# Kernel optimization log

Hardware: AMD Instinct MI355X
Metric: run time of the kernel (lower is better)

Reference implementation:

```python
import jax, jax.numpy as jnp
import numpy as np

B, N, D, P = 4, 4096, 64, 2
M, H = 64, 128
ARENA = 20.0  # positions uniform in [0, ARENA]^2; radius 1.0 -> ~32 neighbors


def _mlp2(x, Wa, ba, Wb, bb):
    return jax.nn.relu(x @ Wa + ba) @ Wb + bb


def setup_inputs() -> dict:
    key = jax.random.key(0)
    ks = jax.random.split(key, 14)
    def lin(k, fan_in, fan_out):
        bound = 1.0 / np.sqrt(fan_in)
        kw, kb = jax.random.split(k)
        W = jax.random.uniform(kw, (fan_in, fan_out), jnp.float32, -bound, bound)
        b = jax.random.uniform(kb, (fan_out,), jnp.float32, -bound, bound)
        return W, b
    W1, b1 = lin(ks[0], D, H)
    W2, b2 = lin(ks[1], H, M)
    W3, b3 = lin(ks[2], 2 * M, H)
    W4, b4 = lin(ks[3], H, M)
    W5, b5 = lin(ks[4], D + M, H)
    W6, b6 = lin(ks[5], H, D)
    agent_states = jax.random.normal(ks[6], (B, N, D), jnp.float32)
    agent_positions = jax.random.uniform(ks[7], (B, N, P), jnp.float32) * ARENA
    return {
        "agent_states": agent_states,
        "agent_positions": agent_positions,
        "neighbor_radius": 1,
        "W1": W1, "b1": b1, "W2": W2, "b2": b2,
        "W3": W3, "b3": b3, "W4": W4, "b4": b4,
        "W5": W5, "b5": b5, "W6": W6, "b6": b6,
    }


def reference(agent_states, agent_positions, neighbor_radius,
              W1, b1, W2, b2, W3, b3, W4, b4, W5, b5, W6, b6):
    n = agent_states.shape[1]
    # message encoder MLP: [B,N,D] -> [B,N,M]
    messages = _mlp2(agent_states, W1, b1, W2, b2)
    # dense pairwise distances [B,N,N] (faithful to original O(N^2) mask)
    diff = agent_positions[:, :, None, :] - agent_positions[:, None, :, :]
    distances = jnp.sqrt(jnp.sum(diff * diff, axis=-1))
    adj = (distances < jnp.float32(neighbor_radius)).astype(messages.dtype)
    adj = adj * (1.0 - jnp.eye(n, dtype=messages.dtype))[None]
    deg = jnp.clip(jnp.sum(adj, axis=-1, keepdims=True), 1.0, None)
    adj = adj / deg
    # vectorized form of the per-agent gather-aggregate loop
    aggregated = jnp.einsum('bij,bjm->bim', adj, messages)
    combined = jnp.concatenate([messages, aggregated], axis=-1)
    final_msgs = _mlp2(combined, W3, b3, W4, b4)
    feats = jnp.concatenate([agent_states, final_msgs], axis=-1)
    out = _mlp2(feats, W5, b5, W6, b6)
    return agent_states + out
```

## Files before the change

kernel.cpp:

```cpp
#include <hip/hip_runtime.h>

typedef unsigned short u16;
typedef __bf16 bf16x8 __attribute__((ext_vector_type(8)));
typedef unsigned short ushort8 __attribute__((ext_vector_type(8)));
typedef float f32x4 __attribute__((ext_vector_type(4)));

#define DEV_INLINE __device__ __forceinline__

constexpr int NB = 4;
constexpr int NAG = 4096;
constexpr int ROWS = NB * NAG;
constexpr int GRID = 20;
constexpr int CELLS = GRID * GRID;
constexpr int CSTRIDE = 404;
constexpr int MAXNB = 320;

DEV_INLINE u16 f2bu(float x) { __bf16 h = (__bf16)x; return __builtin_bit_cast(u16, h); }
DEV_INLINE float bu2f(u16 u) { return __builtin_bit_cast(float, ((unsigned)u) << 16); }

DEV_INLINE f32x4 MF(bf16x8 a, const u16* p, f32x4 c) {
  ushort8 bu = *(const ushort8*)p;
  return __builtin_amdgcn_mfma_f32_16x16x32_bf16(a, __builtin_bit_cast(bf16x8, bu), c, 0, 0, 0);
}

template<bool BF>
DEV_INLINE bf16x8 loadA(const void* __restrict__ src, int row, int c) {
  if constexpr (BF) {
    ushort8 u = *reinterpret_cast<const ushort8*>((const u16*)src + (size_t)row * 64 + c);
    return __builtin_bit_cast(bf16x8, u);
  } else {
    const float* f = (const float*)src + (size_t)row * 64 + c;
    f32x4 a = *(const f32x4*)f;
    f32x4 b = *(const f32x4*)(f + 4);
    bf16x8 r;
    r[0] = (__bf16)a[0]; r[1] = (__bf16)a[1]; r[2] = (__bf16)a[2]; r[3] = (__bf16)a[3];
    r[4] = (__bf16)b[0]; r[5] = (__bf16)b[1]; r[6] = (__bf16)b[2]; r[7] = (__bf16)b[3];
    return r;
  }
}

__global__ __launch_bounds__(256) void fused_setup_mlp1(
    const float* __restrict__ pos, const float* __restrict__ states,
    const float* __restrict__ W1, const float* __restrict__ b1,
    const float* __restrict__ W2, const float* __restrict__ b2,
    const float* __restrict__ W3, const float* __restrict__ W4,
    const float* __restrict__ W5, const float* __restrict__ W6,
    u16* __restrict__ wts, u16* __restrict__ msgs,
    float2* __restrict__ pos_sorted, int* __restrict__ cell_start,
    int* __restrict__ sid)
{
  extern __shared__ u16 smem[];
  const int tid = threadIdx.x;
  const int lane = tid & 63;
  const int wave = tid >> 6;

  if (blockIdx.x < NB) {
    int* cnt_s = (int*)smem;
    int* start_s = cnt_s + CELLS;
    u16* cell_of = (u16*)(start_s + CELLS + 1);
    u16* rank_of = cell_of + NAG;
    const int b = blockIdx.x;
    const float2* pb = (const float2*)(pos + (size_t)b * NAG * 2);
    for (int c = tid; c < CELLS; c += 256) cnt_s[c] = 0;
    __syncthreads();
    for (int i = tid; i < NAG; i += 256) {
      float2 p = pb[i];
      int cx = min(max((int)floorf(p.x), 0), GRID - 1);
      int cy = min(max((int)floorf(p.y), 0), GRID - 1);
      int c = cy * GRID + cx;
      rank_of[i] = (u16)atomicAdd(&cnt_s[c], 1);
      cell_of[i] = (u16)c;
    }
    __syncthreads();
    if (wave == 0) {
      int carry = 0;
      for (int g = 0; g < CELLS; g += 64) {
        int c = g + lane;
        int x = (c < CELLS) ? cnt_s[c] : 0;
#pragma unroll
        for (int off = 1; off < 64; off <<= 1) {
          int y = __shfl_up(x, off, 64);
          if (lane >= off) x += y;
        }
        if (c < CELLS) start_s[c + 1] = carry + x;
        carry += __shfl(x, 63, 64);
      }
      if (lane == 0) start_s[0] = 0;
    }
    __syncthreads();
    for (int c = tid; c <= CELLS; c += 256) cell_start[b * CSTRIDE + c] = start_s[c];
    for (int i = tid; i < NAG; i += 256) {
      int kk = start_s[cell_of[i]] + (int)rank_of[i];
      sid[b * NAG + kk] = b * NAG + i;
      pos_sorted[b * NAG + kk] = pb[i];
    }
    return;
  }

  if (blockIdx.x >= NB + 256) {
    const int base = (blockIdx.x - (NB + 256)) * 3072;
#pragma unroll
    for (int t = 0; t < 12; ++t) {
      int idx = base + t * 256 + tid;
      const float* src; int n, k, Nc;
      if (idx < 16384)      { src = W3; n = idx >> 7; k = idx & 127; Nc = 128; }
      else if (idx < 24576) { int li = idx - 16384; src = W4; n = li >> 7; k = li & 127; Nc = 64; }
      else if (idx < 40960) { int li = idx - 24576; src = W5; n = li >> 7; k = li & 127; Nc = 128; }
      else                  { int li = idx - 40960; src = W6; n = li >> 7; k = li & 127; Nc = 64; }
      wts[idx] = f2bu(src[k * Nc + n]);
    }
    return;
  }

  u16* WaTs = smem;
  u16* WbTs = smem + 128 * 72;
  u16* hs = WbTs + 64 * 136 + wave * (16 * 136);

  for (int e = tid; e < 64 * 128; e += 256) {
    int n = e & 127, k = e >> 7;
    WaTs[n * 72 + k] = f2bu(W1[e]);
  }
  for (int e = tid; e < 128 * 64; e += 256) {
    int n = e & 63, k = e >> 6;
    WbTs[n * 136 + k] = f2bu(W2[e]);
  }
  __syncthreads();

  const int l15 = lane & 15;
  const int khalf = (lane >> 4) * 8;
  const int rb = (blockIdx.x - NB) * 64 + wave * 16;
  const int row = rb + l15;

  f32x4 acc1[8] = {};
#pragma unroll
  for (int kt = 0; kt < 2; ++kt) {
    bf16x8 a = loadA<false>(states, row, kt * 32 + khalf);
#pragma unroll
    for (int nt = 0; nt < 8; ++nt)
      acc1[nt] = MF(a, &WaTs[(nt * 16 + l15) * 72 + kt * 32 + khalf], acc1[nt]);
  }
#pragma unroll
  for (int nt = 0; nt < 8; ++nt) {
    const float bav = b1[nt * 16 + l15];
#pragma unroll
    for (int r = 0; r < 4; ++r)
      hs[((lane >> 4) * 4 + r) * 136 + nt * 16 + l15] = f2bu(fmaxf(acc1[nt][r] + bav, 0.0f));
  }
  f32x4 acc2[4] = {};
#pragma unroll
  for (int kt = 0; kt < 4; ++kt) {
    ushort8 au = *(const ushort8*)&hs[l15 * 136 + kt * 32 + khalf];
    bf16x8 a2 = __builtin_bit_cast(bf16x8, au);
#pragma unroll
    for (int nt = 0; nt < 4; ++nt)
      acc2[nt] = MF(a2, &WbTs[(nt * 16 + l15) * 136 + kt * 32 + khalf], acc2[nt]);
  }
#pragma unroll
  for (int nt = 0; nt < 4; ++nt) {
    const int gc = nt * 16 + l15;
    const float bbv = b2[gc];
#pragma unroll
    for (int r = 0; r < 4; ++r) {
      const int m = (lane >> 4) * 4 + r;
      msgs[(size_t)(rb + m) * 64 + gc] = f2bu(acc2[nt][r] + bbv);
    }
  }
}

__global__ __launch_bounds__(256) void agg_kernel(
    const float2* __restrict__ pos_sorted, const u16* __restrict__ msgs,
    const int* __restrict__ cell_start, const int* __restrict__ sid,
    const int* __restrict__ radius_ptr, u16* __restrict__ aggr)
{
  __shared__ u16 idxb[4][MAXNB];
  const int b = blockIdx.y;
  const int lane = threadIdx.x & 63;
  const int wave = threadIdx.x >> 6;
  const int k = blockIdx.x * 4 + wave;
  const float2* pb = pos_sorted + (size_t)b * NAG;
  const float2 pk = pb[k];
  const float r = (float)(*radius_ptr);
  const float r2 = __fmul_rn(r, r);
  const int cx = min(max((int)floorf(pk.x), 0), GRID - 1);
  const int cy = min(max((int)floorf(pk.y), 0), GRID - 1);
  const int* cs = cell_start + b * CSTRIDE;
  const int* sb = sid + b * NAG;
  const unsigned long long lt = (1ull << lane) - 1ull;

  int cnt = 0;
#pragma unroll
  for (int dy = -1; dy <= 1; ++dy) {
    const int yy = cy + dy;
    if (yy < 0 || yy >= GRID) continue;
    const int x0 = max(cx - 1, 0), x1 = min(cx + 1, GRID - 1);
    const int c0 = cs[yy * GRID + x0];
    const int c1 = cs[yy * GRID + x1 + 1];
    for (int base = c0; base < c1; base += 64) {
      const int j = base + lane;
      bool ok = false;
      if (j < c1) {
        const float2 pj = pb[j];
        const float dx_ = pk.x - pj.x;
        const float dy_ = pk.y - pj.y;
        const float d2 = __fadd_rn(__fmul_rn(dx_, dx_), __fmul_rn(dy_, dy_));
        ok = (d2 < r2) && (j != k);
      }
      const unsigned long long m = __ballot(ok);
      if (ok) {
        const int p = cnt + __popcll(m & lt);
        if (p < MAXNB) idxb[wave][p] = (u16)sb[j];
      }
      cnt += (int)__popcll(m);
    }
  }

  float acc = 0.0f;
  const int n = min(cnt, MAXNB);
  for (int g = 0; g < n; g += 8) {
    ushort8 ii = *(const ushort8*)&idxb[wave][g];
    float vs[8];
#pragma unroll
    for (int s = 0; s < 8; ++s) {
      const int jj = (g + s < n) ? (int)ii[s] : (int)ii[0];
      vs[s] = bu2f(msgs[(size_t)jj * 64 + lane]);
    }
#pragma unroll
    for (int s = 0; s < 8; ++s) acc += (g + s < n) ? vs[s] : 0.0f;
  }
  const float inv = 1.0f / (float)(cnt > 0 ? cnt : 1);
  const int orow = sb[k];
  aggr[(size_t)orow * 64 + lane] = f2bu(acc * inv);
}

__global__ __launch_bounds__(256) void mlp23_kernel(
    const float* __restrict__ states, const u16* __restrict__ msgs,
    const u16* __restrict__ aggr, const u16* __restrict__ wts,
    const float* __restrict__ b3, const float* __restrict__ b4,
    const float* __restrict__ b5, const float* __restrict__ b6,
    float* __restrict__ out)
{
  extern __shared__ u16 smem[];
  u16* W3s = smem;
  u16* W4s = W3s + 128 * 136;
  u16* W5s = W4s + 64 * 136;
  u16* W6s = W5s + 128 * 136;
  const int tid = threadIdx.x;
  const int lane = tid & 63;
  const int wave = tid >> 6;
  u16* hs = W6s + 64 * 136 + wave * (2 * 16 * 136);
  u16* fs = hs + 16 * 136;

  for (int t = tid; t < 2048; t += 256) { int e = t * 8; int n = e >> 7, k = e & 127;
    *(ushort8*)&W3s[n * 136 + k] = *(const ushort8*)&wts[e]; }
  for (int t = tid; t < 1024; t += 256) { int e = t * 8; int n = e >> 7, k = e & 127;
    *(ushort8*)&W4s[n * 136 + k] = *(const ushort8*)&wts[16384 + e]; }
  for (int t = tid; t < 2048; t += 256) { int e = t * 8; int n = e >> 7, k = e & 127;
    *(ushort8*)&W5s[n * 136 + k] = *(const ushort8*)&wts[24576 + e]; }
  for (int t = tid; t < 1024; t += 256) { int e = t * 8; int n = e >> 7, k = e & 127;
    *(ushort8*)&W6s[n * 136 + k] = *(const ushort8*)&wts[40960 + e]; }
  __syncthreads();

  const int l15 = lane & 15;
  const int khalf = (lane >> 4) * 8;
  const int rb = blockIdx.x * 64 + wave * 16;
  const int row = rb + l15;

  f32x4 acc1[8] = {};
#pragma unroll
  for (int kt = 0; kt < 4; ++kt) {
    const int cc = (kt & 1) * 32 + khalf;
    bf16x8 a = (kt < 2) ? loadA<true>(msgs, row, cc) : loadA<true>(aggr, row, cc);
#pragma unroll
    for (int nt = 0; nt < 8; ++nt)
      acc1[nt] = MF(a, &W3s[(nt * 16 + l15) * 136 + kt * 32 + khalf], acc1[nt]);
  }
#pragma unroll
  for (int nt = 0; nt < 8; ++nt) {
    const float bv = b3[nt * 16 + l15];
#pragma unroll
    for (int r = 0; r < 4; ++r)
      hs[((lane >> 4) * 4 + r) * 136 + nt * 16 + l15] = f2bu(fmaxf(acc1[nt][r] + bv, 0.0f));
  }
  f32x4 acc2[4] = {};
#pragma unroll
  for (int kt = 0; kt < 4; ++kt) {
    ushort8 au = *(const ushort8*)&hs[l15 * 136 + kt * 32 + khalf];
    bf16x8 a2 = __builtin_bit_cast(bf16x8, au);
#pragma unroll
    for (int nt = 0; nt < 4; ++nt)
      acc2[nt] = MF(a2, &W4s[(nt * 16 + l15) * 136 + kt * 32 + khalf], acc2[nt]);
  }
#pragma unroll
  for (int nt = 0; nt < 4; ++nt) {
    const int gc = nt * 16 + l15;
    const float bv = b4[gc];
#pragma unroll
    for (int r = 0; r < 4; ++r)
      fs[((lane >> 4) * 4 + r) * 136 + gc] = f2bu(acc2[nt][r] + bv);
  }
  f32x4 acc3[8] = {};
#pragma unroll
  for (int kt = 0; kt < 4; ++kt) {
    const int cc = (kt & 1) * 32 + khalf;
    bf16x8 a;
    if (kt < 2) a = loadA<false>(states, row, cc);
    else {
      ushort8 au = *(const ushort8*)&fs[l15 * 136 + cc];
      a = __builtin_bit_cast(bf16x8, au);
    }
#pragma unroll
    for (int nt = 0; nt < 8; ++nt)
      acc3[nt] = MF(a, &W5s[(nt * 16 + l15) * 136 + kt * 32 + khalf], acc3[nt]);
  }
#pragma unroll
  for (int nt = 0; nt < 8; ++nt) {
    const float bv = b5[nt * 16 + l15];
#pragma unroll
    for (int r = 0; r < 4; ++r)
      hs[((lane >> 4) * 4 + r) * 136 + nt * 16 + l15] = f2bu(fmaxf(acc3[nt][r] + bv, 0.0f));
  }
  f32x4 acc4[4] = {};
#pragma unroll
  for (int kt = 0; kt < 4; ++kt) {
    ushort8 au = *(const ushort8*)&hs[l15 * 136 + kt * 32 + khalf];
    bf16x8 a2 = __builtin_bit_cast(bf16x8, au);
#pragma unroll
    for (int nt = 0; nt < 4; ++nt)
      acc4[nt] = MF(a2, &W6s[(nt * 16 + l15) * 136 + kt * 32 + khalf], acc4[nt]);
  }
#pragma unroll
  for (int nt = 0; nt < 4; ++nt) {
    const int gc = nt * 16 + l15;
    const float bv = b6[gc];
#pragma unroll
    for (int r = 0; r < 4; ++r) {
      const int m = (lane >> 4) * 4 + r;
      const size_t o = (size_t)(rb + m) * 64 + gc;
      out[o] = acc4[nt][r] + bv + states[o];
    }
  }
}

extern "C" void kernel_launch(void* const* d_in, const int* in_sizes, int n_in,
                              void* d_out, int out_size, void* d_ws, size_t ws_size,
                              hipStream_t stream) {
  const float* states = (const float*)d_in[0];
  const float* pos    = (const float*)d_in[1];
  const int*   radius = (const int*)d_in[2];
  const float* W1 = (const float*)d_in[3];
  const float* b1 = (const float*)d_in[4];
  const float* W2 = (const float*)d_in[5];
  const float* b2 = (const float*)d_in[6];
  const float* W3 = (const float*)d_in[7];
  const float* b3 = (const float*)d_in[8];
  const float* W4 = (const float*)d_in[9];
  const float* b4 = (const float*)d_in[10];
  const float* W5 = (const float*)d_in[11];
  const float* b5 = (const float*)d_in[12];
  const float* W6 = (const float*)d_in[13];
  const float* b6 = (const float*)d_in[14];
  float* out = (float*)d_out;

  u16* ws16 = (u16*)d_ws;
  u16* msgs = ws16;
  u16* aggr = msgs + (size_t)ROWS * 64;
  u16* wts  = aggr + (size_t)ROWS * 64;
  char* pbyte = (char*)(wts + 49152);
  float2* pos_sorted = (float2*)pbyte;
  int* cell_start = (int*)(pbyte + (size_t)ROWS * 8);
  int* sid = cell_start + NB * CSTRIDE;

  constexpr int LDS_K1 = (128 * 72 + 64 * 136 + 4 * 16 * 136) * 2;
  constexpr int LDS_K3 = (128 * 136 + 64 * 136 + 128 * 136 + 64 * 136 + 4 * 2 * 16 * 136) * 2;

  fused_setup_mlp1<<<NB + 256 + 16, 256, LDS_K1, stream>>>(
      pos, states, W1, b1, W2, b2, W3, W4, W5, W6,
      wts, msgs, pos_sorted, cell_start, sid);

  agg_kernel<<<dim3(NAG / 4, NB), 256, 0, stream>>>(
      pos_sorted, msgs, cell_start, sid, radius, aggr);

  mlp23_kernel<<<256, 256, LDS_K3, stream>>>(
      states, msgs, aggr, wts, b3, b4, b5, b6, out);
}
```

Measured before the change: 43.38 us.

## Read MLP weights directly from global and split output columns across waves

The final MLP kernel no longer stages all four weight matrices (about 100 KB) in LDS. MFMA B-operands are now read straight from the global transposed bf16 weights, which should hit in L2. Each block handles 32 rows instead of 64, with two wave pairs splitting the output columns of each layer and exchanging activations through small shared buffers and block barriers. The weight pre-transpose write pattern changes so that loads are coalesced while stores scatter. This aims to remove the per-block weight staging cost and raise occupancy and grid size, at the cost of more global/L2 traffic and extra syncs.

```diff
diff --git a/kernel.cpp b/kernel.cpp
--- a/kernel.cpp
+++ b/kernel.cpp
@@ -102,12 +102,12 @@
 #pragma unroll
     for (int t = 0; t < 12; ++t) {
       int idx = base + t * 256 + tid;
-      const float* src; int n, k, Nc;
-      if (idx < 16384)      { src = W3; n = idx >> 7; k = idx & 127; Nc = 128; }
-      else if (idx < 24576) { int li = idx - 16384; src = W4; n = li >> 7; k = li & 127; Nc = 64; }
-      else if (idx < 40960) { int li = idx - 24576; src = W5; n = li >> 7; k = li & 127; Nc = 128; }
-      else                  { int li = idx - 40960; src = W6; n = li >> 7; k = li & 127; Nc = 64; }
-      wts[idx] = f2bu(src[k * Nc + n]);
+      const float* src; int e, k, n, dst;
+      if (idx < 16384)      { src = W3; e = idx;         k = e >> 7; n = e & 127; dst = n * 128 + k; }
+      else if (idx < 24576) { src = W4; e = idx - 16384; k = e >> 6; n = e & 63;  dst = 16384 + n * 128 + k; }
+      else if (idx < 40960) { src = W5; e = idx - 24576; k = e >> 7; n = e & 127; dst = 24576 + n * 128 + k; }
+      else                  { src = W6; e = idx - 40960; k = e >> 6; n = e & 63;  dst = 40960 + n * 128 + k; }
+      wts[dst] = f2bu(src[e]);
     }
     return;
   }
@@ -239,104 +239,116 @@
     const float* __restrict__ b5, const float* __restrict__ b6,
     float* __restrict__ out)
 {
-  extern __shared__ u16 smem[];
-  u16* W3s = smem;
-  u16* W4s = W3s + 128 * 136;
-  u16* W5s = W4s + 64 * 136;
-  u16* W6s = W5s + 128 * 136;
+  __shared__ u16 hs[2][16 * 136];
+  __shared__ u16 fs[2][16 * 136];
   const int tid = threadIdx.x;
   const int lane = tid & 63;
   const int wave = tid >> 6;
-  u16* hs = W6s + 64 * 136 + wave * (2 * 16 * 136);
-  u16* fs = hs + 16 * 136;
-
-  for (int t = tid; t < 2048; t += 256) { int e = t * 8; int n = e >> 7, k = e & 127;
-    *(ushort8*)&W3s[n * 136 + k] = *(const ushort8*)&wts[e]; }
-  for (int t = tid; t < 1024; t += 256) { int e = t * 8; int n = e >> 7, k = e & 127;
-    *(ushort8*)&W4s[n * 136 + k] = *(const ushort8*)&wts[16384 + e]; }
-  for (int t = tid; t < 2048; t += 256) { int e = t * 8; int n = e >> 7, k = e & 127;
-    *(ushort8*)&W5s[n * 136 + k] = *(const ushort8*)&wts[24576 + e]; }
-  for (int t = tid; t < 1024; t += 256) { int e = t * 8; int n = e >> 7, k = e & 127;
-    *(ushort8*)&W6s[n * 136 + k] = *(const ushort8*)&wts[40960 + e]; }
-  __syncthreads();
-
+  const int g = wave & 1;
+  const int ch = wave >> 1;
   const int l15 = lane & 15;
   const int khalf = (lane >> 4) * 8;
-  const int rb = blockIdx.x * 64 + wave * 16;
+  const int rb = blockIdx.x * 32 + g * 16;
   const int row = rb + l15;
 
-  f32x4 acc1[8] = {};
+  const u16* W3T = wts;
+  const u16* W4T = wts + 16384;
+  const u16* W5T = wts + 24576;
+  const u16* W6T = wts + 40960;
+
+  bf16x8 a1[4];
 #pragma unroll
   for (int kt = 0; kt < 4; ++kt) {
     const int cc = (kt & 1) * 32 + khalf;
-    bf16x8 a = (kt < 2) ? loadA<true>(msgs, row, cc) : loadA<true>(aggr, row, cc);
-#pragma unroll
-    for (int nt = 0; nt < 8; ++nt)
-      acc1[nt] = MF(a, &W3s[(nt * 16 + l15) * 136 + kt * 32 + khalf], acc1[nt]);
-  }
-#pragma unroll
-  for (int nt = 0; nt < 8; ++nt) {
-    const float bv = b3[nt * 16 + l15];
+    a1[kt] = (kt < 2) ? loadA<true>(msgs, row, cc) : loadA<true>(aggr, row, cc);
+  }
+  f32x4 acc1[4] = {};
+#pragma unroll
+  for (int kt = 0; kt < 4; ++kt) {
+#pragma unroll
+    for (int j = 0; j < 4; ++j) {
+      const int nt = ch * 4 + j;
+      acc1[j] = MF(a1[kt], &W3T[(nt * 16 + l15) * 128 + kt * 32 + khalf], acc1[j]);
+    }
+  }
+#pragma unroll
+  for (int j = 0; j < 4; ++j) {
+    const int col = (ch * 4 + j) * 16 + l15;
+    const float bv = b3[col];
 #pragma unroll
     for (int r = 0; r < 4; ++r)
-      hs[((lane >> 4) * 4 + r) * 136 + nt * 16 + l15] = f2bu(fmaxf(acc1[nt][r] + bv, 0.0f));
-  }
-  f32x4 acc2[4] = {};
-#pragma unroll
-  for (int kt = 0; kt < 4; ++kt) {
-    ushort8 au = *(const ushort8*)&hs[l15 * 136 + kt * 32 + khalf];
+      hs[g][((lane >> 4) * 4 + r) * 136 + col] = f2bu(fmaxf(acc1[j][r] + bv, 0.0f));
+  }
+  __syncthreads();
+
+  f32x4 acc2[2] = {};
+#pragma unroll
+  for (int kt = 0; kt < 4; ++kt) {
+    ushort8 au = *(const ushort8*)&hs[g][l15 * 136 + kt * 32 + khalf];
     bf16x8 a2 = __builtin_bit_cast(bf16x8, au);
 #pragma unroll
-    for (int nt = 0; nt < 4; ++nt)
-      acc2[nt] = MF(a2, &W4s[(nt * 16 + l15) * 136 + kt * 32 + khalf], acc2[nt]);
-  }
-#pragma unroll
-  for (int nt = 0; nt < 4; ++nt) {
-    const int gc = nt * 16 + l15;
-    const float bv = b4[gc];
+    for (int j = 0; j < 2; ++j) {
+      const int nt = ch * 2 + j;
+      acc2[j] = MF(a2, &W4T[(nt * 16 + l15) * 128 + kt * 32 + khalf], acc2[j]);
+    }
+  }
+#pragma unroll
+  for (int j = 0; j < 2; ++j) {
+    const int col = (ch * 2 + j) * 16 + l15;
+    const float bv = b4[col];
 #pragma unroll
     for (int r = 0; r < 4; ++r)
-      fs[((lane >> 4) * 4 + r) * 136 + gc] = f2bu(acc2[nt][r] + bv);
-  }
-  f32x4 acc3[8] = {};
+      fs[g][((lane >> 4) * 4 + r) * 136 + col] = f2bu(acc2[j][r] + bv);
+  }
+  __syncthreads();
+
+  f32x4 acc3[4] = {};
 #pragma unroll
   for (int kt = 0; kt < 4; ++kt) {
     const int cc = (kt & 1) * 32 + khalf;
     bf16x8 a;
     if (kt < 2) a = loadA<false>(states, row, cc);
     else {
-      ushort8 au = *(const ushort8*)&fs[l15 * 136 + cc];
+      ushort8 au = *(const ushort8*)&fs[g][l15 * 136 + cc];
       a = __builtin_bit_cast(bf16x8, au);
     }
 #pragma unroll
-    for (int nt = 0; nt < 8; ++nt)
-      acc3[nt] = MF(a, &W5s[(nt * 16 + l15) * 136 + kt * 32 + khalf], acc3[nt]);
-  }
-#pragma unroll
-  for (int nt = 0; nt < 8; ++nt) {
-    const float bv = b5[nt * 16 + l15];
+    for (int j = 0; j < 4; ++j) {
+      const int nt = ch * 4 + j;
+      acc3[j] = MF(a, &W5T[(nt * 16 + l15) * 128 + kt * 32 + khalf], acc3[j]);
+    }
+  }
+  __syncthreads();
+#pragma unroll
+  for (int j = 0; j < 4; ++j) {
+    const int col = (ch * 4 + j) * 16 + l15;
+    const float bv = b5[col];
 #pragma unroll
     for (int r = 0; r < 4; ++r)
-      hs[((lane >> 4) * 4 + r) * 136 + nt * 16 + l15] = f2bu(fmaxf(acc3[nt][r] + bv, 0.0f));
-  }
-  f32x4 acc4[4] = {};
-#pragma unroll
-  for (int kt = 0; kt < 4; ++kt) {
-    ushort8 au = *(const ushort8*)&hs[l15 * 136 + kt * 32 + khalf];
+      hs[g][((lane >> 4) * 4 + r) * 136 + col] = f2bu(fmaxf(acc3[j][r] + bv, 0.0f));
+  }
+  __syncthreads();
+
+  f32x4 acc4[2] = {};
+#pragma unroll
+  for (int kt = 0; kt < 4; ++kt) {
+    ushort8 au = *(const ushort8*)&hs[g][l15 * 136 + kt * 32 + khalf];
     bf16x8 a2 = __builtin_bit_cast(bf16x8, au);
 #pragma unroll
-    for (int nt = 0; nt < 4; ++nt)
-      acc4[nt] = MF(a2, &W6s[(nt * 16 + l15) * 136 + kt * 32 + khalf], acc4[nt]);
-  }
-#pragma unroll
-  for (int nt = 0; nt < 4; ++nt) {
-    const int gc = nt * 16 + l15;
-    const float bv = b6[gc];
+    for (int j = 0; j < 2; ++j) {
+      const int nt = ch * 2 + j;
+      acc4[j] = MF(a2, &W6T[(nt * 16 + l15) * 128 + kt * 32 + khalf], acc4[j]);
+    }
+  }
+#pragma unroll
+  for (int j = 0; j < 2; ++j) {
+    const int col = (ch * 2 + j) * 16 + l15;
+    const float bv = b6[col];
 #pragma unroll
     for (int r = 0; r < 4; ++r) {
       const int m = (lane >> 4) * 4 + r;
-      const size_t o = (size_t)(rb + m) * 64 + gc;
-      out[o] = acc4[nt][r] + bv + states[o];
+      const size_t o = (size_t)(rb + m) * 64 + col;
+      out[o] = acc4[j][r] + bv + states[o];
     }
   }
 }
@@ -371,7 +383,6 @@
   int* sid = cell_start + NB * CSTRIDE;
 
   constexpr int LDS_K1 = (128 * 72 + 64 * 136 + 4 * 16 * 136) * 2;
-  constexpr int LDS_K3 = (128 * 136 + 64 * 136 + 128 * 136 + 64 * 136 + 4 * 2 * 16 * 136) * 2;
 
   fused_setup_mlp1<<<NB + 256 + 16, 256, LDS_K1, stream>>>(
       pos, states, W1, b1, W2, b2, W3, W4, W5, W6,
@@ -380,6 +391,6 @@
   agg_kernel<<<dim3(NAG / 4, NB), 256, 0, stream>>>(
       pos_sorted, msgs, cell_start, sid, radius, aggr);
 
-  mlp23_kernel<<<256, 256, LDS_K3, stream>>>(
+  mlp23_kernel<<<ROWS / 32, 256, 0, stream>>>(
       states, msgs, aggr, wts, b3, b4, b5, b6, out);
 }
```

After: 50.79 us. 1.17x slower.

## Split MLP23 columns across 16 waves per block and prefetch activations before weight staging

Applied to the files above, without the earlier changes.

The final MLP kernel moves from 4 waves per block, each computing all output columns for 16 rows, to 16 waves per block, where four waves share a 16-row group and each computes a quarter of the columns. Intermediate activations go through shared LDS with block-wide barriers between layers. Activation loads (msgs, aggr, states) are issued before the weight staging loop in both the first and last kernels, so their global latency overlaps with the LDS fill. This adds four __syncthreads per block and needs 1024 threads per block, which may limit how many blocks run at once; the register cost per thread falls.

```diff
diff --git a/kernel.cpp b/kernel.cpp
--- a/kernel.cpp
+++ b/kernel.cpp
@@ -116,28 +116,31 @@
   u16* WbTs = smem + 128 * 72;
   u16* hs = WbTs + 64 * 136 + wave * (16 * 136);
 
-  for (int e = tid; e < 64 * 128; e += 256) {
-    int n = e & 127, k = e >> 7;
-    WaTs[n * 72 + k] = f2bu(W1[e]);
-  }
-  for (int e = tid; e < 128 * 64; e += 256) {
-    int n = e & 63, k = e >> 6;
-    WbTs[n * 136 + k] = f2bu(W2[e]);
-  }
-  __syncthreads();
-
   const int l15 = lane & 15;
   const int khalf = (lane >> 4) * 8;
   const int rb = (blockIdx.x - NB) * 64 + wave * 16;
   const int row = rb + l15;
 
+  bf16x8 aS[2];
+  aS[0] = loadA<false>(states, row, khalf);
+  aS[1] = loadA<false>(states, row, 32 + khalf);
+
+  for (int e = tid; e < 64 * 128; e += 256) {
+    int n = e & 127, k = e >> 7;
+    WaTs[n * 72 + k] = f2bu(W1[e]);
+  }
+  for (int e = tid; e < 128 * 64; e += 256) {
+    int n = e & 63, k = e >> 6;
+    WbTs[n * 136 + k] = f2bu(W2[e]);
+  }
+  __syncthreads();
+
   f32x4 acc1[8] = {};
 #pragma unroll
   for (int kt = 0; kt < 2; ++kt) {
-    bf16x8 a = loadA<false>(states, row, kt * 32 + khalf);
 #pragma unroll
     for (int nt = 0; nt < 8; ++nt)
-      acc1[nt] = MF(a, &WaTs[(nt * 16 + l15) * 72 + kt * 32 + khalf], acc1[nt]);
+      acc1[nt] = MF(aS[kt], &WaTs[(nt * 16 + l15) * 72 + kt * 32 + khalf], acc1[nt]);
   }
 #pragma unroll
   for (int nt = 0; nt < 8; ++nt) {
@@ -232,7 +235,7 @@
   aggr[(size_t)orow * 64 + lane] = f2bu(acc * inv);
 }
 
-__global__ __launch_bounds__(256) void mlp23_kernel(
+__global__ __launch_bounds__(1024, 4) void mlp23_kernel(
     const float* __restrict__ states, const u16* __restrict__ msgs,
     const u16* __restrict__ aggr, const u16* __restrict__ wts,
     const float* __restrict__ b3, const float* __restrict__ b4,
@@ -244,99 +247,117 @@
   u16* W4s = W3s + 128 * 136;
   u16* W5s = W4s + 64 * 136;
   u16* W6s = W5s + 128 * 136;
+  u16* hsb = W6s + 64 * 136;
+  u16* fsb = hsb + 4 * 16 * 136;
+
   const int tid = threadIdx.x;
   const int lane = tid & 63;
   const int wave = tid >> 6;
-  u16* hs = W6s + 64 * 136 + wave * (2 * 16 * 136);
-  u16* fs = hs + 16 * 136;
-
-  for (int t = tid; t < 2048; t += 256) { int e = t * 8; int n = e >> 7, k = e & 127;
-    *(ushort8*)&W3s[n * 136 + k] = *(const ushort8*)&wts[e]; }
-  for (int t = tid; t < 1024; t += 256) { int e = t * 8; int n = e >> 7, k = e & 127;
-    *(ushort8*)&W4s[n * 136 + k] = *(const ushort8*)&wts[16384 + e]; }
-  for (int t = tid; t < 2048; t += 256) { int e = t * 8; int n = e >> 7, k = e & 127;
-    *(ushort8*)&W5s[n * 136 + k] = *(const ushort8*)&wts[24576 + e]; }
-  for (int t = tid; t < 1024; t += 256) { int e = t * 8; int n = e >> 7, k = e & 127;
-    *(ushort8*)&W6s[n * 136 + k] = *(const ushort8*)&wts[40960 + e]; }
-  __syncthreads();
-
+  const int rg = wave >> 2;
+  const int cq = wave & 3;
   const int l15 = lane & 15;
   const int khalf = (lane >> 4) * 8;
-  const int rb = blockIdx.x * 64 + wave * 16;
+  const int rb = blockIdx.x * 64 + rg * 16;
   const int row = rb + l15;
-
-  f32x4 acc1[8] = {};
+  u16* hs = hsb + rg * (16 * 136);
+  u16* fs = fsb + rg * (16 * 136);
+
+  bf16x8 aM[2], aG[2], aS[2];
+  aM[0] = loadA<true>(msgs, row, khalf);
+  aM[1] = loadA<true>(msgs, row, 32 + khalf);
+  aG[0] = loadA<true>(aggr, row, khalf);
+  aG[1] = loadA<true>(aggr, row, 32 + khalf);
+  aS[0] = loadA<false>(states, row, khalf);
+  aS[1] = loadA<false>(states, row, 32 + khalf);
+
+  for (int t = tid; t < 6144; t += 1024) {
+    const int e = t * 8;
+    ushort8 v = *(const ushort8*)&wts[e];
+    u16* dst;
+    if (e < 16384)      dst = &W3s[(e >> 7) * 136 + (e & 127)];
+    else if (e < 24576) { int li = e - 16384; dst = &W4s[(li >> 7) * 136 + (li & 127)]; }
+    else if (e < 40960) { int li = e - 24576; dst = &W5s[(li >> 7) * 136 + (li & 127)]; }
+    else                { int li = e - 40960; dst = &W6s[(li >> 7) * 136 + (li & 127)]; }
+    *(ushort8*)dst = v;
+  }
+  __syncthreads();
+
+  f32x4 acc1[2] = {};
 #pragma unroll
   for (int kt = 0; kt < 4; ++kt) {
-    const int cc = (kt & 1) * 32 + khalf;
-    bf16x8 a = (kt < 2) ? loadA<true>(msgs, row, cc) : loadA<true>(aggr, row, cc);
-#pragma unroll
-    for (int nt = 0; nt < 8; ++nt)
-      acc1[nt] = MF(a, &W3s[(nt * 16 + l15) * 136 + kt * 32 + khalf], acc1[nt]);
-  }
-#pragma unroll
-  for (int nt = 0; nt < 8; ++nt) {
-    const float bv = b3[nt * 16 + l15];
+    bf16x8 a = (kt < 2) ? aM[kt] : aG[kt - 2];
+#pragma unroll
+    for (int j = 0; j < 2; ++j) {
+      const int nt = cq * 2 + j;
+      acc1[j] = MF(a, &W3s[(nt * 16 + l15) * 136 + kt * 32 + khalf], acc1[j]);
+    }
+  }
+#pragma unroll
+  for (int j = 0; j < 2; ++j) {
+    const int col = (cq * 2 + j) * 16 + l15;
+    const float bv = b3[col];
 #pragma unroll
     for (int r = 0; r < 4; ++r)
-      hs[((lane >> 4) * 4 + r) * 136 + nt * 16 + l15] = f2bu(fmaxf(acc1[nt][r] + bv, 0.0f));
-  }
-  f32x4 acc2[4] = {};
+      hs[((lane >> 4) * 4 + r) * 136 + col] = f2bu(fmaxf(acc1[j][r] + bv, 0.0f));
+  }
+  __syncthreads();
+
+  f32x4 acc2 = {};
 #pragma unroll
   for (int kt = 0; kt < 4; ++kt) {
     ushort8 au = *(const ushort8*)&hs[l15 * 136 + kt * 32 + khalf];
-    bf16x8 a2 = __builtin_bit_cast(bf16x8, au);
-#pragma unroll
-    for (int nt = 0; nt < 4; ++nt)
-      acc2[nt] = MF(a2, &W4s[(nt * 16 + l15) * 136 + kt * 32 + khalf], acc2[nt]);
-  }
-#pragma unroll
-  for (int nt = 0; nt < 4; ++nt) {
-    const int gc = nt * 16 + l15;
-    const float bv = b4[gc];
+    acc2 = MF(__builtin_bit_cast(bf16x8, au),
+              &W4s[(cq * 16 + l15) * 136 + kt * 32 + khalf], acc2);
+  }
+  {
+    const int col = cq * 16 + l15;
+    const float bv = b4[col];
 #pragma unroll
     for (int r = 0; r < 4; ++r)
-      fs[((lane >> 4) * 4 + r) * 136 + gc] = f2bu(acc2[nt][r] + bv);
-  }
-  f32x4 acc3[8] = {};
+      fs[((lane >> 4) * 4 + r) * 136 + col] = f2bu(acc2[r] + bv);
+  }
+  __syncthreads();
+
+  f32x4 acc3[2] = {};
 #pragma unroll
   for (int kt = 0; kt < 4; ++kt) {
-    const int cc = (kt & 1) * 32 + khalf;
     bf16x8 a;
-    if (kt < 2) a = loadA<false>(states, row, cc);
+    if (kt < 2) a = aS[kt];
     else {
-      ushort8 au = *(const ushort8*)&fs[l15 * 136 + cc];
+      ushort8 au = *(const ushort8*)&fs[l15 * 136 + (kt - 2) * 32 + khalf];
       a = __builtin_bit_cast(bf16x8, au);
     }
 #pragma unroll
-    for (int nt = 0; nt < 8; ++nt)
-      acc3[nt] = MF(a, &W5s[(nt * 16 + l15) * 136 + kt * 32 + khalf], acc3[nt]);
-  }
-#pragma unroll
-  for (int nt = 0; nt < 8; ++nt) {
-    const float bv = b5[nt * 16 + l15];
+    for (int j = 0; j < 2; ++j) {
+      const int nt = cq * 2 + j;
+      acc3[j] = MF(a, &W5s[(nt * 16 + l15) * 136 + kt * 32 + khalf], acc3[j]);
+    }
+  }
+#pragma unroll
+  for (int j = 0; j < 2; ++j) {
+    const int col = (cq * 2 + j) * 16 + l15;
+    const float bv = b5[col];
 #pragma unroll
     for (int r = 0; r < 4; ++r)
-      hs[((lane >> 4) * 4 + r) * 136 + nt * 16 + l15] = f2bu(fmaxf(acc3[nt][r] + bv, 0.0f));
-  }
-  f32x4 acc4[4] = {};
+      hs[((lane >> 4) * 4 + r) * 136 + col] = f2bu(fmaxf(acc3[j][r] + bv, 0.0f));
+  }
+  __syncthreads();
+
+  f32x4 acc4 = {};
 #pragma unroll
   for (int kt = 0; kt < 4; ++kt) {
     ushort8 au = *(const ushort8*)&hs[l15 * 136 + kt * 32 + khalf];
-    bf16x8 a2 = __builtin_bit_cast(bf16x8, au);
-#pragma unroll
-    for (int nt = 0; nt < 4; ++nt)
-      acc4[nt] = MF(a2, &W6s[(nt * 16 + l15) * 136 + kt * 32 + khalf], acc4[nt]);
-  }
-#pragma unroll
-  for (int nt = 0; nt < 4; ++nt) {
-    const int gc = nt * 16 + l15;
-    const float bv = b6[gc];
+    acc4 = MF(__builtin_bit_cast(bf16x8, au),
+              &W6s[(cq * 16 + l15) * 136 + kt * 32 + khalf], acc4);
+  }
+  {
+    const int col = cq * 16 + l15;
+    const float bv = b6[col];
 #pragma unroll
     for (int r = 0; r < 4; ++r) {
       const int m = (lane >> 4) * 4 + r;
-      const size_t o = (size_t)(rb + m) * 64 + gc;
-      out[o] = acc4[nt][r] + bv + states[o];
+      const size_t o = (size_t)(rb + m) * 64 + col;
+      out[o] = acc4[r] + bv + states[o];
     }
   }
 }
@@ -371,7 +392,7 @@
   int* sid = cell_start + NB * CSTRIDE;
 
   constexpr int LDS_K1 = (128 * 72 + 64 * 136 + 4 * 16 * 136) * 2;
-  constexpr int LDS_K3 = (128 * 136 + 64 * 136 + 128 * 136 + 64 * 136 + 4 * 2 * 16 * 136) * 2;
+  constexpr int LDS_K3 = (384 * 136 + 8 * 16 * 136) * 2;
 
   fused_setup_mlp1<<<NB + 256 + 16, 256, LDS_K1, stream>>>(
       pos, states, W1, b1, W2, b2, W3, W4, W5, W6,
@@ -380,6 +401,6 @@
   agg_kernel<<<dim3(NAG / 4, NB), 256, 0, stream>>>(
       pos_sorted, msgs, cell_start, sid, radius, aggr);
 
-  mlp23_kernel<<<256, 256, LDS_K3, stream>>>(
+  mlp23_kernel<<<ROWS / 64, 1024, LDS_K3, stream>>>(
       states, msgs, aggr, wts, b3, b4, b5, b6, out);
 }
```

Result: faster. 42.34 us (-2.4%).
